# Performance work log

Hardware: AMD Instinct MI355X
Metric: run time of the kernel (lower is better)

The kernel has to match this reference:

```python
import jax, jax.numpy as jnp
import numpy as np

NUM_GRAPHS = 1024
DIM = 64
IN_DIM = 25
PROC_STEPS = 3


def setup_inputs() -> dict:
    key = jax.random.key(0)
    ks = jax.random.split(key, 14)
    N, E = 100000, 1600000
    s = 0.1
    x = jax.random.normal(ks[0], (N, IN_DIM), jnp.float32)
    edge_index = jax.random.randint(ks[1], (2, E), 0, N, dtype=jnp.int64)
    batch = jnp.sort(jax.random.randint(ks[2], (N,), 0, NUM_GRAPHS, dtype=jnp.int64))
    return {
        "x": x,
        "edge_index": edge_index,
        "batch": batch,
        # lin0: 25 -> 64
        "lin0_W": jax.random.normal(ks[3], (IN_DIM, DIM), jnp.float32) * s,
        "lin0_b": jnp.zeros((DIM,), jnp.float32),
        # GINConv nn: 64 -> 64
        "gin_W": jax.random.normal(ks[4], (DIM, DIM), jnp.float32) * s,
        "gin_b": jnp.zeros((DIM,), jnp.float32),
        # Set2Set LSTM: input 2*dim -> hidden dim, torch gate order (i, f, g, o)
        "W_ih": jax.random.normal(ks[5], (4 * DIM, 2 * DIM), jnp.float32) * s,
        "W_hh": jax.random.normal(ks[6], (4 * DIM, DIM), jnp.float32) * s,
        "b_ih": jnp.zeros((4 * DIM,), jnp.float32),
        "b_hh": jnp.zeros((4 * DIM,), jnp.float32),
        # lin1: 128 -> 64, lin2: 64 -> 1
        "lin1_W": jax.random.normal(ks[7], (2 * DIM, DIM), jnp.float32) * s,
        "lin1_b": jnp.zeros((DIM,), jnp.float32),
        "lin2_W": jax.random.normal(ks[8], (DIM, 1), jnp.float32) * s,
        "lin2_b": jnp.zeros((1,), jnp.float32),
    }


def reference(x, edge_index, batch, lin0_W, lin0_b, gin_W, gin_b,
              W_ih, W_hh, b_ih, b_hh, lin1_W, lin1_b, lin2_W, lin2_b):
    N = x.shape[0]
    B = NUM_GRAPHS
    # lin0 + relu
    h0 = jax.nn.relu(x @ lin0_W + lin0_b)  # [N, 64]
    # GINConv (eps=0): out = nn((1+eps)*x + sum_{j in N(i)} x_j), then relu
    src, dst = edge_index[0], edge_index[1]
    aggr = jax.ops.segment_sum(h0[src], dst, num_segments=N)  # scatter-add [N, 64]
    h1 = jax.nn.relu((h0 + aggr) @ gin_W + gin_b)  # [N, 64]
    # Set2Set pooling: 3 steps of LSTM + softmax attention over each graph
    q_star = jnp.zeros((B, 2 * DIM), h1.dtype)
    h = jnp.zeros((B, DIM), h1.dtype)
    c = jnp.zeros((B, DIM), h1.dtype)
    for _ in range(PROC_STEPS):
        gates = q_star @ W_ih.T + h @ W_hh.T + b_ih + b_hh  # [B, 4*64]
        i_g, f_g, g_g, o_g = jnp.split(gates, 4, axis=-1)
        c = jax.nn.sigmoid(f_g) * c + jax.nn.sigmoid(i_g) * jnp.tanh(g_g)
        h = jax.nn.sigmoid(o_g) * jnp.tanh(c)
        q = h  # query [B, 64]
        e = jnp.sum(h1 * q[batch], axis=-1)  # [N]
        e_max = jax.ops.segment_max(e, batch, num_segments=B)
        a_un = jnp.exp(e - e_max[batch])
        denom = jax.ops.segment_sum(a_un, batch, num_segments=B)
        denom = jnp.where(denom == 0, 1.0, denom)
        a = a_un / denom[batch]  # per-graph softmax over nodes
        r = jax.ops.segment_sum(a[:, None] * h1, batch, num_segments=B)  # [B, 64]
        q_star = jnp.concatenate([q, r], axis=-1)  # [B, 128]
    out = jax.nn.relu(q_star @ lin1_W + lin1_b)
    out = out @ lin2_W + lin2_b  # [B, 1]
    return out.reshape(-1)
```

## Files before the change

kernel.cpp:

```cpp
#include <hip/hip_runtime.h>
#include <hip/hip_fp16.h>
#include <math.h>

#define DIM 64
#define IN_DIM 25
#define B_GRAPHS 1024
#define STEPS 3
#define MAXDEG 64
#define GPB 4
#define SPANCAP 544
#define SCCAP 160
#define BSHIFT 9
#define NBUCK_MAX 256
#define BCAP 10240
#define CHUNK_A 4096

typedef _Float16 half8 __attribute__((ext_vector_type(8)));
typedef float    f32x4 __attribute__((ext_vector_type(4)));

__device__ __forceinline__ float wave_sum(float v) {
    #pragma unroll
    for (int o = 32; o > 0; o >>= 1) v += __shfl_xor(v, o, 64);
    return v;
}

__global__ void prepA_kernel(const int* __restrict__ ei, int E,
                             int* __restrict__ gcur,
                             unsigned* __restrict__ arena, int nbuck) {
    __shared__ int hist[NBUCK_MAX];
    int tid = threadIdx.x;
    for (int t = tid; t < nbuck; t += 256) hist[t] = 0;
    __syncthreads();
    int e0 = blockIdx.x * CHUNK_A;
    int dstr[16], lofs[16];
    #pragma unroll
    for (int k = 0; k < 16; ++k) {
        int e = e0 + k * 256 + tid;
        dstr[k] = -1;
        if (e < E) {
            int d = ei[E + e];
            dstr[k] = d;
            lofs[k] = atomicAdd(&hist[d >> BSHIFT], 1);
        }
    }
    __syncthreads();
    for (int t = tid; t < nbuck; t += 256)
        hist[t] = atomicAdd(&gcur[t], hist[t]);
    __syncthreads();
    #pragma unroll
    for (int k = 0; k < 16; ++k) {
        int d = dstr[k];
        if (d >= 0) {
            int e = e0 + k * 256 + tid;
            unsigned src = (unsigned)ei[e];
            int bk = d >> BSHIFT;
            int pos = hist[bk] + lofs[k];
            if (pos < BCAP)
                arena[(size_t)bk * BCAP + pos] =
                    (src << BSHIFT) | (unsigned)(d & ((1 << BSHIFT) - 1));
        }
    }
}

__global__ void prepB_kernel(const float* __restrict__ x,
                             const float* __restrict__ W,
                             const float* __restrict__ b,
                             __half* __restrict__ h0h,
                             const int* __restrict__ batch, int N,
                             const unsigned* __restrict__ arena,
                             const int* __restrict__ gcur,
                             int* __restrict__ cnt, int* __restrict__ csr,
                             int* __restrict__ startb, int* __restrict__ endb,
                             int nbuck, int nbL) {
    int bi = blockIdx.x;
    if (bi < nbuck) {
        int tid = threadIdx.x;
        __shared__ int cur[1 << BSHIFT];
        for (int t = tid; t < (1 << BSHIFT); t += 256) cur[t] = 0;
        __syncthreads();
        int nE = gcur[bi];
        if (nE > BCAP) nE = BCAP;
        int base = bi << BSHIFT;
        const unsigned* ap = arena + (size_t)bi * BCAP;
        for (int i = tid; i < nE; i += 256) {
            unsigned pk = ap[i];
            int dl  = pk & ((1 << BSHIFT) - 1);
            int src = pk >> BSHIFT;
            int pos = atomicAdd(&cur[dl], 1);
            if (pos < MAXDEG) {
                int slot = (pos & 3) * 16 + (pos >> 2);
                csr[(size_t)(base + dl) * MAXDEG + slot] = src;
            }
        }
        __syncthreads();
        for (int t = tid; t < (1 << BSHIFT); t += 256) {
            int d = base + t;
            if (d < N) cnt[d] = cur[t] < MAXDEG ? cur[t] : MAXDEG;
        }
    } else if (bi < nbuck + nbL) {
        int grp  = threadIdx.x >> 6;
        int lane = threadIdx.x & 63;
        int n = (bi - nbuck) * 4 + grp;
        if (n >= N) return;
        float acc = b[lane];
        const float* xr = x + (size_t)n * IN_DIM;
        #pragma unroll
        for (int k = 0; k < IN_DIM; ++k)
            acc += xr[k] * W[k * DIM + lane];
        h0h[(size_t)n * DIM + lane] = __float2half(fmaxf(acc, 0.f));
    } else {
        int i = (bi - nbuck - nbL) * 256 + threadIdx.x;
        if (i >= N) return;
        int g = batch[i];
        if (i == 0) {
            startb[g] = 0;
        } else if (batch[i - 1] != g) {
            startb[g] = i;
            endb[batch[i - 1]] = i;
        }
        if (i == N - 1) endb[g] = N;
    }
}

__global__ void gin_gather_kernel(const __half* __restrict__ h0h,
                                  const int* __restrict__ cnt,
                                  const int* __restrict__ csr,
                                  const float* __restrict__ W,
                                  const float* __restrict__ bias,
                                  __half* __restrict__ h1h, int N) {
    int wid  = threadIdx.x >> 6;
    int lane = threadIdx.x & 63;
    int sub  = lane & 15;
    int quad = lane >> 4;
    int nbase = blockIdx.x * 16;
    __shared__ __align__(16) __half agg[16][72];

    half8 bfrag0, bfrag1;
    {
        int cb = wid * 16 + sub;
        #pragma unroll
        for (int j = 0; j < 8; ++j) {
            bfrag0[j] = (_Float16)W[(quad * 8 + j) * DIM + cb];
            bfrag1[j] = (_Float16)W[(32 + quad * 8 + j) * DIM + cb];
        }
    }
    float bias_l = bias[wid * 16 + sub];

    #pragma unroll
    for (int t = 0; t < 4; ++t) {
        int n = nbase + t * 4 + wid;
        if (n < N) {
            int d = cnt[n];
            const int4* crow = (const int4*)(csr + (size_t)n * MAXDEG + quad * 16);
            int4 c0 = crow[0];
            float4 a0 = {0.f, 0.f, 0.f, 0.f};
            float4 a1 = {0.f, 0.f, 0.f, 0.f};

            bool v0 = (0 + quad) < d,  v1 = (4 + quad) < d;
            bool v2 = (8 + quad) < d,  v3 = (12 + quad) < d;
            int i0 = v0 ? c0.x : 0, i1 = v1 ? c0.y : 0;
            int i2 = v2 ? c0.z : 0, i3 = v3 ? c0.w : 0;
            uint2 r0 = *(const uint2*)(h0h + (size_t)i0 * DIM + 4 * sub);
            uint2 r1 = *(const uint2*)(h0h + (size_t)i1 * DIM + 4 * sub);
            uint2 r2 = *(const uint2*)(h0h + (size_t)i2 * DIM + 4 * sub);
            uint2 r3 = *(const uint2*)(h0h + (size_t)i3 * DIM + 4 * sub);
            #define ACC8(r, v, A)                                              \
                if (v) {                                                       \
                    __half2 ua = *reinterpret_cast<__half2*>(&(r).x);          \
                    __half2 ub = *reinterpret_cast<__half2*>(&(r).y);          \
                    float2 fa = __half22float2(ua), fb = __half22float2(ub);   \
                    A.x += fa.x; A.y += fa.y; A.z += fb.x; A.w += fb.y;        \
                }
            ACC8(r0, v0, a0) ACC8(r1, v1, a1) ACC8(r2, v2, a0) ACC8(r3, v3, a1)

            if (d > 16) {
                int4 c1 = crow[1];
                bool v4 = (16 + quad) < d, v5 = (20 + quad) < d;
                bool v6 = (24 + quad) < d, v7 = (28 + quad) < d;
                int i4 = v4 ? c1.x : 0, i5 = v5 ? c1.y : 0;
                int i6 = v6 ? c1.z : 0, i7 = v7 ? c1.w : 0;
                uint2 r4 = *(const uint2*)(h0h + (size_t)i4 * DIM + 4 * sub);
                uint2 r5 = *(const uint2*)(h0h + (size_t)i5 * DIM + 4 * sub);
                uint2 r6 = *(const uint2*)(h0h + (size_t)i6 * DIM + 4 * sub);
                uint2 r7 = *(const uint2*)(h0h + (size_t)i7 * DIM + 4 * sub);
                ACC8(r4, v4, a0) ACC8(r5, v5, a1) ACC8(r6, v6, a0) ACC8(r7, v7, a1)
            }
            if (d > 32) {
                int4 c2 = crow[2];
                int4 c3 = crow[3];
                bool w0 = (32 + quad) < d, w1 = (36 + quad) < d;
                bool w2 = (40 + quad) < d, w3 = (44 + quad) < d;
                bool w4 = (48 + quad) < d, w5 = (52 + quad) < d;
                bool w6 = (56 + quad) < d, w7 = (60 + quad) < d;
                int k0 = w0 ? c2.x : 0, k1 = w1 ? c2.y : 0;
                int k2 = w2 ? c2.z : 0, k3 = w3 ? c2.w : 0;
                int k4 = w4 ? c3.x : 0, k5 = w5 ? c3.y : 0;
                int k6 = w6 ? c3.z : 0, k7 = w7 ? c3.w : 0;
                uint2 t0 = *(const uint2*)(h0h + (size_t)k0 * DIM + 4 * sub);
                uint2 t1 = *(const uint2*)(h0h + (size_t)k1 * DIM + 4 * sub);
                uint2 t2 = *(const uint2*)(h0h + (size_t)k2 * DIM + 4 * sub);
                uint2 t3 = *(const uint2*)(h0h + (size_t)k3 * DIM + 4 * sub);
                uint2 t4 = *(const uint2*)(h0h + (size_t)k4 * DIM + 4 * sub);
                uint2 t5 = *(const uint2*)(h0h + (size_t)k5 * DIM + 4 * sub);
                uint2 t6 = *(const uint2*)(h0h + (size_t)k6 * DIM + 4 * sub);
                uint2 t7 = *(const uint2*)(h0h + (size_t)k7 * DIM + 4 * sub);
                ACC8(t0, w0, a0) ACC8(t1, w1, a1) ACC8(t2, w2, a0) ACC8(t3, w3, a1)
                ACC8(t4, w4, a0) ACC8(t5, w5, a1) ACC8(t6, w6, a0) ACC8(t7, w7, a1)
            }
            #undef ACC8

            float4 a;
            a.x = a0.x + a1.x; a.y = a0.y + a1.y;
            a.z = a0.z + a1.z; a.w = a0.w + a1.w;
            a.x += __shfl_xor(a.x, 16, 64); a.y += __shfl_xor(a.y, 16, 64);
            a.z += __shfl_xor(a.z, 16, 64); a.w += __shfl_xor(a.w, 16, 64);
            a.x += __shfl_xor(a.x, 32, 64); a.y += __shfl_xor(a.y, 32, 64);
            a.z += __shfl_xor(a.z, 32, 64); a.w += __shfl_xor(a.w, 32, 64);
            if (quad == 0) {
                const __half2* p = (const __half2*)(h0h + (size_t)n * DIM + 4 * sub);
                float2 f0 = __half22float2(p[0]), f1 = __half22float2(p[1]);
                a.x += f0.x; a.y += f0.y; a.z += f1.x; a.w += f1.y;
                __half2* dp = (__half2*)&agg[t * 4 + wid][4 * sub];
                dp[0] = __floats2half2_rn(a.x, a.y);
                dp[1] = __floats2half2_rn(a.z, a.w);
            }
        }
    }
    __syncthreads();

    half8 afrag0 = *(const half8*)&agg[sub][quad * 8];
    half8 afrag1 = *(const half8*)&agg[sub][32 + quad * 8];
    f32x4 acc = {0.f, 0.f, 0.f, 0.f};
    acc = __builtin_amdgcn_mfma_f32_16x16x32_f16(afrag0, bfrag0, acc, 0, 0, 0);
    acc = __builtin_amdgcn_mfma_f32_16x16x32_f16(afrag1, bfrag1, acc, 0, 0, 0);
    #pragma unroll
    for (int r = 0; r < 4; ++r) {
        int n = nbase + quad * 4 + r;
        if (n < N) {
            float v = fmaxf(acc[r] + bias_l, 0.f);
            h1h[(size_t)n * DIM + wid * 16 + sub] = __float2half(v);
        }
    }
}

__global__ __launch_bounds__(256)
void set2set_fused_kernel(const __half* __restrict__ h1h,
                          const float* __restrict__ W_ih,
                          const float* __restrict__ W_hh,
                          const float* __restrict__ b_ih,
                          const float* __restrict__ b_hh,
                          const int* __restrict__ startb,
                          const int* __restrict__ endb,
                          const float* __restrict__ lin1_W,
                          const float* __restrict__ lin1_b,
                          const float* __restrict__ lin2_W,
                          const float* __restrict__ lin2_b,
                          float* __restrict__ out) {
    int g0  = blockIdx.x * GPB;
    int tid = threadIdx.x;
    __shared__ __align__(16) __half sh1[SPANCAP * DIM];
    __shared__ __align__(16) float qsbuf[GPB][2 * DIM];
    __shared__ float csbuf[GPB][DIM];
    __shared__ float gatesL[GPB][4 * DIM];
    __shared__ float scL[GPB][SCCAP];

    int myg  = tid >> 6;
    int lane = tid & 63;
    int st0  = startb[g0];
    int stg  = startb[g0 + myg];
    int cntg = endb[g0 + myg] - stg;
    if (cntg < 0) cntg = 0;
    int lb   = stg - st0;
    int span = endb[g0 + GPB - 1] - st0;
    if (span < 0) span = 0;
    int stage = span < SPANCAP ? span : SPANCAP;

    {
        const uint2* src = (const uint2*)(h1h + (size_t)st0 * DIM);
        uint2* dst = (uint2*)sh1;
        for (int f = tid; f < stage * 16; f += 256) dst[f] = src[f];
    }
    for (int f = tid; f < GPB * 2 * DIM; f += 256) ((float*)qsbuf)[f] = 0.f;
    for (int f = tid; f < GPB * DIM; f += 256) ((float*)csbuf)[f] = 0.f;
    float bias_t = b_ih[tid] + b_hh[tid];
    __syncthreads();

    int sub   = lane & 15;
    int jslot = lane >> 4;

    for (int step = 0; step < STEPS; ++step) {
        {
            float a0 = bias_t, a1 = bias_t, a2 = bias_t, a3 = bias_t;
            const float4* wi = (const float4*)(W_ih + (size_t)tid * 2 * DIM);
            const float4* q0 = (const float4*)qsbuf[0];
            const float4* q1 = (const float4*)qsbuf[1];
            const float4* q2 = (const float4*)qsbuf[2];
            const float4* q3 = (const float4*)qsbuf[3];
            #pragma unroll 4
            for (int k = 0; k < 2 * DIM / 4; ++k) {
                float4 w = wi[k];
                float4 v0 = q0[k], v1 = q1[k], v2 = q2[k], v3 = q3[k];
                a0 += w.x * v0.x + w.y * v0.y + w.z * v0.z + w.w * v0.w;
                a1 += w.x * v1.x + w.y * v1.y + w.z * v1.z + w.w * v1.w;
                a2 += w.x * v2.x + w.y * v2.y + w.z * v2.z + w.w * v2.w;
                a3 += w.x * v3.x + w.y * v3.y + w.z * v3.z + w.w * v3.w;
            }
            const float4* wh = (const float4*)(W_hh + (size_t)tid * DIM);
            #pragma unroll 4
            for (int k = 0; k < DIM / 4; ++k) {
                float4 w = wh[k];
                float4 v0 = q0[k], v1 = q1[k], v2 = q2[k], v3 = q3[k];
                a0 += w.x * v0.x + w.y * v0.y + w.z * v0.z + w.w * v0.w;
                a1 += w.x * v1.x + w.y * v1.y + w.z * v1.z + w.w * v1.w;
                a2 += w.x * v2.x + w.y * v2.y + w.z * v2.z + w.w * v2.w;
                a3 += w.x * v3.x + w.y * v3.y + w.z * v3.z + w.w * v3.w;
            }
            gatesL[0][tid] = a0; gatesL[1][tid] = a1;
            gatesL[2][tid] = a2; gatesL[3][tid] = a3;
        }
        __syncthreads();
        {
            int g = myg, d = lane;
            float ig = gatesL[g][d];
            float fg = gatesL[g][DIM + d];
            float gg = gatesL[g][2 * DIM + d];
            float og = gatesL[g][3 * DIM + d];
            float si = 1.f / (1.f + __expf(-ig));
            float sf = 1.f / (1.f + __expf(-fg));
            float so = 1.f / (1.f + __expf(-og));
            float cn = sf * csbuf[g][d] + si * tanhf(gg);
            float hn = so * tanhf(cn);
            csbuf[g][d] = cn;
            qsbuf[g][d] = hn;
        }
        __syncthreads();

        const float4 q4 = *(const float4*)(&qsbuf[myg][4 * sub]);

        float gmax = -INFINITY;
        for (int i = jslot; i < cntg; i += 4) {
            int r = lb + i;
            const __half2* p = (r < stage)
                ? (const __half2*)(sh1 + (size_t)r * DIM + 4 * sub)
                : (const __half2*)(h1h + (size_t)(stg + i) * DIM + 4 * sub);
            float2 f0 = __half22float2(p[0]), f1 = __half22float2(p[1]);
            float pdot = f0.x * q4.x + f0.y * q4.y + f1.x * q4.z + f1.y * q4.w;
            pdot += __shfl_xor(pdot, 1, 64);
            pdot += __shfl_xor(pdot, 2, 64);
            pdot += __shfl_xor(pdot, 4, 64);
            pdot += __shfl_xor(pdot, 8, 64);
            if (sub == 0 && i < SCCAP) scL[myg][i] = pdot;
            gmax = fmaxf(gmax, pdot);
        }
        gmax = fmaxf(gmax, __shfl_xor(gmax, 16, 64));
        gmax = fmaxf(gmax, __shfl_xor(gmax, 32, 64));
        float m = gmax;

        float4 racc = {0.f, 0.f, 0.f, 0.f};
        float den = 0.f;
        for (int i = jslot; i < cntg; i += 4) {
            int r = lb + i;
            const __half2* p = (r < stage)
                ? (const __half2*)(sh1 + (size_t)r * DIM + 4 * sub)
                : (const __half2*)(h1h + (size_t)(stg + i) * DIM + 4 * sub);
            float2 f0 = __half22float2(p[0]), f1 = __half22float2(p[1]);
            float pdot;
            if (i < SCCAP) {
                pdot = scL[myg][i];
            } else {
                pdot = f0.x * q4.x + f0.y * q4.y + f1.x * q4.z + f1.y * q4.w;
                pdot += __shfl_xor(pdot, 1, 64);
                pdot += __shfl_xor(pdot, 2, 64);
                pdot += __shfl_xor(pdot, 4, 64);
                pdot += __shfl_xor(pdot, 8, 64);
            }
            float w = __expf(pdot - m);
            if (sub == 0) den += w;
            racc.x += w * f0.x; racc.y += w * f0.y; racc.z += w * f1.x; racc.w += w * f1.y;
        }
        racc.x += __shfl_xor(racc.x, 16, 64); racc.y += __shfl_xor(racc.y, 16, 64);
        racc.z += __shfl_xor(racc.z, 16, 64); racc.w += __shfl_xor(racc.w, 16, 64);
        racc.x += __shfl_xor(racc.x, 32, 64); racc.y += __shfl_xor(racc.y, 32, 64);
        racc.z += __shfl_xor(racc.z, 32, 64); racc.w += __shfl_xor(racc.w, 32, 64);
        den += __shfl_xor(den, 16, 64);
        den += __shfl_xor(den, 32, 64);
        float dt = __shfl(den, 0, 64);
        if (dt == 0.f) dt = 1.f;
        if (jslot == 0) {
            float4 rv;
            rv.x = racc.x / dt; rv.y = racc.y / dt;
            rv.z = racc.z / dt; rv.w = racc.w / dt;
            *(float4*)(&qsbuf[myg][DIM + 4 * sub]) = rv;
        }
        __syncthreads();
    }

    {
        float acc = lin1_b[lane];
        const float* qv = qsbuf[myg];
        #pragma unroll 8
        for (int k = 0; k < 2 * DIM; ++k)
            acc += qv[k] * lin1_W[k * DIM + lane];
        acc = fmaxf(acc, 0.f);
        float v = acc * lin2_W[lane];
        v = wave_sum(v);
        if (lane == 0) out[g0 + myg] = v + lin2_b[0];
    }
}

extern "C" void kernel_launch(void* const* d_in, const int* in_sizes, int n_in,
                              void* d_out, int out_size, void* d_ws, size_t ws_size,
                              hipStream_t stream) {
    const float* x      = (const float*)d_in[0];
    const int*   ei     = (const int*)d_in[1];
    const int*   batch  = (const int*)d_in[2];
    const float* lin0_W = (const float*)d_in[3];
    const float* lin0_b = (const float*)d_in[4];
    const float* gin_W  = (const float*)d_in[5];
    const float* gin_b  = (const float*)d_in[6];
    const float* W_ih   = (const float*)d_in[7];
    const float* W_hh   = (const float*)d_in[8];
    const float* b_ih   = (const float*)d_in[9];
    const float* b_hh   = (const float*)d_in[10];
    const float* lin1_W = (const float*)d_in[11];
    const float* lin1_b = (const float*)d_in[12];
    const float* lin2_W = (const float*)d_in[13];
    const float* lin2_b = (const float*)d_in[14];
    float* out = (float*)d_out;

    const int N = in_sizes[2];
    const int E = in_sizes[1] / 2;

    char* ws = (char*)d_ws;
    size_t off = 0;
    auto take = [&](size_t bytes) -> char* {
        char* p = ws + off;
        off += (bytes + 255) & ~(size_t)255;
        return p;
    };
    int nbuck = (N + (1 << BSHIFT) - 1) >> BSHIFT;

    __half*   h0h   = (__half*)take((size_t)N * DIM * 2);
    __half*   h1h   = (__half*)take((size_t)N * DIM * 2);
    int*      csr   = (int*)take((size_t)N * MAXDEG * 4);
    unsigned* arena = (unsigned*)take((size_t)nbuck * BCAP * 4);
    int*      cnt   = (int*)take((size_t)N * 4);
    int* startb = (int*)take((size_t)B_GRAPHS * 4);
    int* endb   = (int*)take((size_t)B_GRAPHS * 4);
    int* gcur   = (int*)take((size_t)NBUCK_MAX * 4);
    size_t zero_bytes = (size_t)((char*)gcur - (char*)startb) + NBUCK_MAX * 4;
    hipMemsetAsync(startb, 0, zero_bytes, stream);

    int nb4   = (N + 3) / 4;
    int nb16  = (N + 15) / 16;
    int nb256 = (N + 255) / 256;
    int fillB = (E + CHUNK_A - 1) / CHUNK_A;

    hipLaunchKernelGGL(prepA_kernel, dim3(fillB), dim3(256), 0, stream,
                       ei, E, gcur, arena, nbuck);
    hipLaunchKernelGGL(prepB_kernel, dim3(nbuck + nb4 + nb256), dim3(256), 0, stream,
                       x, lin0_W, lin0_b, h0h, batch, N,
                       arena, gcur, cnt, csr, startb, endb, nbuck, nb4);
    hipLaunchKernelGGL(gin_gather_kernel, dim3(nb16), dim3(256), 0, stream,
                       h0h, cnt, csr, gin_W, gin_b, h1h, N);
    hipLaunchKernelGGL(set2set_fused_kernel, dim3(B_GRAPHS / GPB), dim3(256), 0, stream,
                       h1h, W_ih, W_hh, b_ih, b_hh, startb, endb,
                       lin1_W, lin1_b, lin2_W, lin2_b, out);
}
```

Before: 281.7 us.

## Stage CSR buckets in LDS for coalesced writes; drop set2set h1 staging

New measurement: 287.0 us. No clear change (+1.9%).

```diff
diff --git a/kernel.cpp b/kernel.cpp
--- a/kernel.cpp
+++ b/kernel.cpp
@@ -8,11 +8,10 @@
 #define STEPS 3
 #define MAXDEG 64
 #define GPB 4
-#define SPANCAP 544
 #define SCCAP 160
-#define BSHIFT 9
-#define NBUCK_MAX 256
-#define BCAP 10240
+#define BSHIFT 7
+#define NBUCK_MAX 1024
+#define BCAP 3072
 #define CHUNK_A 4096
 
 typedef _Float16 half8 __attribute__((ext_vector_type(8)));
@@ -76,6 +75,7 @@
     if (bi < nbuck) {
         int tid = threadIdx.x;
         __shared__ int cur[1 << BSHIFT];
+        __shared__ int stage[(1 << BSHIFT) * MAXDEG];
         for (int t = tid; t < (1 << BSHIFT); t += 256) cur[t] = 0;
         __syncthreads();
         int nE = gcur[bi];
@@ -89,14 +89,18 @@
             int pos = atomicAdd(&cur[dl], 1);
             if (pos < MAXDEG) {
                 int slot = (pos & 3) * 16 + (pos >> 2);
-                csr[(size_t)(base + dl) * MAXDEG + slot] = src;
+                stage[dl * MAXDEG + slot] = src;
             }
         }
         __syncthreads();
-        for (int t = tid; t < (1 << BSHIFT); t += 256) {
-            int d = base + t;
-            if (d < N) cnt[d] = cur[t] < MAXDEG ? cur[t] : MAXDEG;
-        }
+        int rows = N - base;
+        if (rows > (1 << BSHIFT)) rows = 1 << BSHIFT;
+        if (rows < 0) rows = 0;
+        const int4* s4 = (const int4*)stage;
+        int4* g4 = (int4*)(csr + (size_t)base * MAXDEG);
+        for (int f = tid; f < rows * 16; f += 256) g4[f] = s4[f];
+        for (int t = tid; t < rows; t += 256)
+            cnt[base + t] = cur[t] < MAXDEG ? cur[t] : MAXDEG;
     } else if (bi < nbuck + nbL) {
         int grp  = threadIdx.x >> 6;
         int lane = threadIdx.x & 63;
@@ -258,7 +262,6 @@
                           float* __restrict__ out) {
     int g0  = blockIdx.x * GPB;
     int tid = threadIdx.x;
-    __shared__ __align__(16) __half sh1[SPANCAP * DIM];
     __shared__ __align__(16) float qsbuf[GPB][2 * DIM];
     __shared__ float csbuf[GPB][DIM];
     __shared__ float gatesL[GPB][4 * DIM];
@@ -266,20 +269,10 @@
 
     int myg  = tid >> 6;
     int lane = tid & 63;
-    int st0  = startb[g0];
     int stg  = startb[g0 + myg];
     int cntg = endb[g0 + myg] - stg;
     if (cntg < 0) cntg = 0;
-    int lb   = stg - st0;
-    int span = endb[g0 + GPB - 1] - st0;
-    if (span < 0) span = 0;
-    int stage = span < SPANCAP ? span : SPANCAP;
-
-    {
-        const uint2* src = (const uint2*)(h1h + (size_t)st0 * DIM);
-        uint2* dst = (uint2*)sh1;
-        for (int f = tid; f < stage * 16; f += 256) dst[f] = src[f];
-    }
+
     for (int f = tid; f < GPB * 2 * DIM; f += 256) ((float*)qsbuf)[f] = 0.f;
     for (int f = tid; f < GPB * DIM; f += 256) ((float*)csbuf)[f] = 0.f;
     float bias_t = b_ih[tid] + b_hh[tid];
@@ -339,10 +332,8 @@
 
         float gmax = -INFINITY;
         for (int i = jslot; i < cntg; i += 4) {
-            int r = lb + i;
-            const __half2* p = (r < stage)
-                ? (const __half2*)(sh1 + (size_t)r * DIM + 4 * sub)
-                : (const __half2*)(h1h + (size_t)(stg + i) * DIM + 4 * sub);
+            const __half2* p =
+                (const __half2*)(h1h + (size_t)(stg + i) * DIM + 4 * sub);
             float2 f0 = __half22float2(p[0]), f1 = __half22float2(p[1]);
             float pdot = f0.x * q4.x + f0.y * q4.y + f1.x * q4.z + f1.y * q4.w;
             pdot += __shfl_xor(pdot, 1, 64);
@@ -359,10 +350,8 @@
         float4 racc = {0.f, 0.f, 0.f, 0.f};
         float den = 0.f;
         for (int i = jslot; i < cntg; i += 4) {
-            int r = lb + i;
-            const __half2* p = (r < stage)
-                ? (const __half2*)(sh1 + (size_t)r * DIM + 4 * sub)
-                : (const __half2*)(h1h + (size_t)(stg + i) * DIM + 4 * sub);
+            const __half2* p =
+                (const __half2*)(h1h + (size_t)(stg + i) * DIM + 4 * sub);
             float2 f0 = __half22float2(p[0]), f1 = __half22float2(p[1]);
             float pdot;
             if (i < SCCAP) {
```
